# Kernel tuning notes

Hardware: AMD Instinct MI355X
Metric: run time of the kernel (lower is better)

Reference implementation:

```python
import jax, jax.numpy as jnp
import numpy as np

B, T, C, H = 8, 2048, 1024, 128  # batch, seq (== block_size), n_embd, head_size


def setup_inputs() -> dict:
    key = jax.random.key(0)
    ks = jax.random.split(key, 4)
    s = 1.0 / np.sqrt(C)  # keep logits sane for softmax
    return {
        "embedded_data": jax.random.normal(ks[0], (B, T, C), dtype=jnp.float32),
        "Wq": jax.random.normal(ks[1], (C, H), dtype=jnp.float32) * s,
        "bq": jnp.zeros((H,), dtype=jnp.float32),
        "Wk": jax.random.normal(ks[2], (C, H), dtype=jnp.float32) * s,
        "bk": jnp.zeros((H,), dtype=jnp.float32),
        "Wv": jax.random.normal(ks[3], (C, H), dtype=jnp.float32) * s,
        "bv": jnp.zeros((H,), dtype=jnp.float32),
    }


def reference(embedded_data, Wq, bq, Wk, bk, Wv, bv):
    Bc, Tc, Cc = embedded_data.shape
    q = embedded_data @ Wq + bq                      # [B,T,H]
    k = embedded_data @ Wk + bk                      # [B,T,H]
    v = embedded_data @ Wv + bv                      # [B,T,H]
    # NOTE: source scales by C**-0.5 (input embed dim), not head_size**-0.5
    wei = jnp.einsum("bqh,bkh->bqk", q, k) * (Cc ** -0.5)  # [B,T,T]
    causal = jnp.tril(jnp.ones((Tc, Tc), dtype=bool))
    wei = jnp.where(causal, wei, -jnp.inf)
    wei = jax.nn.softmax(wei, axis=-1)
    # dropout(p=0.2) is identity in eval mode
    out = jnp.einsum("bqk,bkh->bqh", wei, v)         # [B,T,H]
    return out
```

## Files before the change

### kernel.cpp

```cpp
#include <hip/hip_runtime.h>
#include <cstdint>
#include <cstddef>

typedef __bf16 bf16x8 __attribute__((ext_vector_type(8)));
typedef float f32x4 __attribute__((ext_vector_type(4)));

#define B_ 8
#define T_ 2048
#define C_ 1024
#define H_ 128

#define QSC 0.045084220027780106f

__device__ __forceinline__ unsigned short f2bf(float f) {
    __bf16 h = (__bf16)f;
    return *(unsigned short*)&h;
}
__device__ __forceinline__ float bf2f(unsigned short u) {
    union { unsigned int i; float f; } x; x.i = ((unsigned int)u) << 16;
    return x.f;
}

__device__ __forceinline__ void gload16(void* lds, const void* g) {
    __builtin_amdgcn_global_load_lds(
        (const __attribute__((address_space(1))) unsigned int*)g,
        (__attribute__((address_space(3))) unsigned int*)lds, 16, 0, 0);
}

__global__ __launch_bounds__(256) void prep_w(
    const float* __restrict__ Wq, const float* __restrict__ Wk,
    const float* __restrict__ Wv, unsigned short* __restrict__ wt)
{
    int gid = blockIdx.x * 256 + threadIdx.x;
    int which = gid >> 14;
    int rem = gid & 16383;
    int n = rem >> 7;
    int kc = rem & 127;
    const float* W = which == 0 ? Wq : (which == 1 ? Wk : Wv);
    unsigned short tmp[8];
    #pragma unroll
    for (int i = 0; i < 8; ++i) tmp[i] = f2bf(W[(size_t)(kc * 8 + i) * H_ + n]);
    *(uint4*)&wt[((size_t)which * H_ + n) * C_ + kc * 8] = *(uint4*)tmp;
}

__global__ __launch_bounds__(512, 2) void proj_fused(
    const float* __restrict__ x, const unsigned short* __restrict__ wt,
    const float* __restrict__ bq, const float* __restrict__ bk,
    const float* __restrict__ bv,
    unsigned short* __restrict__ qo, unsigned short* __restrict__ ko,
    unsigned short* __restrict__ vo)
{
    __shared__ float xs[2][64 * 64];
    __shared__ unsigned short ws2[2][384 * 64];

    const int tid = threadIdx.x;
    const int w = tid >> 6, l = tid & 63, gl = l >> 4, lc = l & 15;
    const int rb = (w >> 1) * 16;
    const int cb = (w & 1) * 192;
    const int m0 = blockIdx.x * 64;

    f32x4 acc[12];
    #pragma unroll
    for (int jn = 0; jn < 12; ++jn) acc[jn] = f32x4{0.f, 0.f, 0.f, 0.f};

    auto stage = [&](int buf, int kc2) {
        const int kb = kc2 * 64;
        #pragma unroll
        for (int ji = 0; ji < 6; ++ji) {
            int slot = ji * 512 + tid;
            int R = slot >> 3, cs = slot & 7;
            gload16(&ws2[buf][(ji * 512 + w * 64) * 8],
                    &wt[(size_t)R * C_ + kb + ((cs ^ (R & 7)) * 8)]);
        }
        #pragma unroll
        for (int ji = 0; ji < 2; ++ji) {
            int slot = ji * 512 + tid;
            int r = slot >> 4, cs = slot & 15;
            gload16(&xs[buf][(ji * 512 + w * 64) * 4],
                    &x[(size_t)(m0 + r) * C_ + kb + ((cs ^ (r & 15)) * 4)]);
        }
    };

    stage(0, 0);
    __syncthreads();

    int cur = 0;
    for (int kc = 0; kc < 16; ++kc) {
        if (kc < 15) stage(cur ^ 1, kc + 1);
        #pragma unroll
        for (int ks = 0; ks < 2; ++ks) {
            const int row = rb + lc;
            const int u0 = ks * 8 + gl * 2;
            f32x4 lo = *(const f32x4*)&xs[cur][(row * 16 + (u0 ^ (row & 15))) * 4];
            f32x4 hi = *(const f32x4*)&xs[cur][(row * 16 + ((u0 + 1) ^ (row & 15))) * 4];
            bf16x8 af;
            af[0] = (__bf16)lo[0]; af[1] = (__bf16)lo[1];
            af[2] = (__bf16)lo[2]; af[3] = (__bf16)lo[3];
            af[4] = (__bf16)hi[0]; af[5] = (__bf16)hi[1];
            af[6] = (__bf16)hi[2]; af[7] = (__bf16)hi[3];
            #pragma unroll
            for (int jn = 0; jn < 12; ++jn) {
                int R = cb + jn * 16 + lc;
                bf16x8 bfr = *(const bf16x8*)&ws2[cur][(R * 8 + ((ks * 4 + gl) ^ (R & 7))) * 8];
                acc[jn] = __builtin_amdgcn_mfma_f32_16x16x32_bf16(af, bfr, acc[jn], 0, 0, 0);
            }
        }
        __syncthreads();
        cur ^= 1;
    }

    unsigned short* eb = (unsigned short*)&ws2[0][0];
    #pragma unroll
    for (int jn = 0; jn < 12; ++jn) {
        int n = cb + jn * 16 + lc;
        int wh = n >> 7, nl = n & 127;
        float bb = (wh == 0) ? bq[nl] : (wh == 1 ? bk[nl] : bv[nl]);
        float sc = (wh == 0) ? QSC : 1.0f;
        #pragma unroll
        for (int r = 0; r < 4; ++r) {
            int row = rb + gl * 4 + r;
            eb[row * 392 + n] = f2bf((acc[jn][r] + bb) * sc);
        }
    }
    __syncthreads();

    const int bi = m0 >> 11, t0 = m0 & (T_ - 1);
    #pragma unroll
    for (int i = 0; i < 2; ++i) {
        int c = i * 512 + tid;
        {
            int row = c >> 4, c16 = c & 15;
            *(uint4*)&qo[(size_t)(m0 + row) * H_ + c16 * 8] =
                *(const uint4*)&eb[row * 392 + c16 * 8];
            *(uint4*)&ko[(size_t)(m0 + row) * H_ + c16 * 8] =
                *(const uint4*)&eb[row * 392 + 128 + c16 * 8];
        }
        {
            int n = c >> 3, cc = c & 7;
            unsigned short tmp[8];
            #pragma unroll
            for (int ii = 0; ii < 8; ++ii)
                tmp[ii] = eb[(cc * 8 + ii) * 392 + 256 + n];
            *(uint4*)&vo[((size_t)(bi * H_ + n)) * T_ + t0 + cc * 8] = *(uint4*)tmp;
        }
    }
}

__device__ __forceinline__ int pasc(int qt) {
    int m = qt >> 2, j = qt & 3;
    return 2 * m * (m + 1) + j * (m + 1);
}

__global__ __launch_bounds__(256, 2) void attn_split7(
    const unsigned short* __restrict__ q,
    const unsigned short* __restrict__ k,
    const unsigned short* __restrict__ vT,
    float* __restrict__ out,
    unsigned short* __restrict__ Opart, float* __restrict__ lws)
{
    const int bb = blockIdx.x;
    const int jj = 143 - (int)blockIdx.y;
    int qt = 31;
    while (pasc(qt) > jj) --qt;
    const int c = jj - pasc(qt);
    const int nch = (qt >> 2) + 1;
    const int q0 = qt * 64;
    const int kstart = c * 256;
    const int kend = min(kstart + 256, q0 + 64);
    const int ntiles = (kend - kstart) >> 5;

    const unsigned short* qb = q  + (size_t)bb * T_ * H_;
    const unsigned short* kb = k  + (size_t)bb * T_ * H_;
    const unsigned short* vb = vT + (size_t)bb * H_ * T_;

    __shared__ unsigned short Ks[2][32 * 128];
    __shared__ unsigned short Vs[2][128 * 32];
    __shared__ unsigned short Ps[4][16 * 64];

    const int tid = threadIdx.x;
    const int w = tid >> 6, l = tid & 63, gl = l >> 4, lc = l & 15;
    const int rowbase = q0 + w * 16;

    bf16x8 aq[4];
    #pragma unroll
    for (int ds = 0; ds < 4; ++ds)
        aq[ds] = *(const bf16x8*)&qb[(size_t)(rowbase + lc) * H_ + ds * 32 + gl * 8];

    f32x4 o[8];
    #pragma unroll
    for (int jo = 0; jo < 8; ++jo) o[jo] = f32x4{0.f, 0.f, 0.f, 0.f};
    float l_acc[4];
    #pragma unroll
    for (int r = 0; r < 4; ++r) l_acc[r] = 0.f;

    auto stageK = [&](int buf, int t) {
        const int kv0 = kstart + t * 32;
        #pragma unroll
        for (int ji = 0; ji < 2; ++ji) {
            int slot = (w * 2 + ji) * 64 + l;
            int r = slot >> 4, cs = slot & 15;
            gload16(&Ks[buf][((w * 2 + ji) * 64) * 8],
                    &kb[(size_t)(kv0 + r) * H_ + ((cs ^ (r & 7)) * 8)]);
        }
    };
    auto stageV = [&](int buf, int t) {
        const int kv0 = kstart + t * 32;
        #pragma unroll
        for (int ji = 0; ji < 2; ++ji) {
            int slot = (w * 2 + ji) * 64 + l;
            int r = slot >> 2, cs = slot & 3;
            gload16(&Vs[buf][((w * 2 + ji) * 64) * 8],
                    &vb[(size_t)r * T_ + kv0 + ((cs ^ (r & 3)) * 8)]);
        }
    };

    stageK(0, 0);
    stageV(0, 0);
    __syncthreads();

    int cur = 0;
    for (int t = 0; t < ntiles; ++t) {
        if (t + 1 < ntiles) { stageK(cur ^ 1, t + 1); stageV(cur ^ 1, t + 1); }
        const int kv0 = kstart + t * 32;
        const bool active = kv0 < rowbase + 16;
        if (active) {
            f32x4 s[2];
            #pragma unroll
            for (int jk = 0; jk < 2; ++jk) s[jk] = f32x4{0.f, 0.f, 0.f, 0.f};
            #pragma unroll
            for (int ds = 0; ds < 4; ++ds) {
                #pragma unroll
                for (int jk = 0; jk < 2; ++jk) {
                    int row = jk * 16 + lc;
                    bf16x8 kf = *(const bf16x8*)&Ks[cur][(row * 16 + ((ds * 4 + gl) ^ (row & 7))) * 8];
                    s[jk] = __builtin_amdgcn_mfma_f32_16x16x32_bf16(aq[ds], kf, s[jk], 0, 0, 0);
                }
            }
            if (kv0 + 31 > rowbase) {
                #pragma unroll
                for (int jk = 0; jk < 2; ++jk)
                    #pragma unroll
                    for (int r = 0; r < 4; ++r)
                        if (kv0 + jk * 16 + lc > rowbase + gl * 4 + r) s[jk][r] = -1e30f;
            }
            #pragma unroll
            for (int jk = 0; jk < 2; ++jk)
                #pragma unroll
                for (int r = 0; r < 4; ++r) {
                    float p = exp2f(fminf(s[jk][r], 80.f));
                    s[jk][r] = p;
                    l_acc[r] += p;
                }
            #pragma unroll
            for (int jk = 0; jk < 2; ++jk)
                #pragma unroll
                for (int r = 0; r < 4; ++r) {
                    int row = gl * 4 + r;
                    Ps[w][(row * 64 + jk * 16 + lc) ^ ((row & 7) << 3)] = f2bf(s[jk][r]);
                }
            {
                bf16x8 pa = *(const bf16x8*)&Ps[w][(lc * 64 + gl * 8) ^ ((lc & 7) << 3)];
                #pragma unroll
                for (int jo = 0; jo < 8; ++jo) {
                    int d = jo * 16 + lc;
                    bf16x8 vf = *(const bf16x8*)&Vs[cur][(d * 4 + (gl ^ (d & 3))) * 8];
                    o[jo] = __builtin_amdgcn_mfma_f32_16x16x32_bf16(pa, vf, o[jo], 0, 0, 0);
                }
            }
        }
        __syncthreads();
        cur ^= 1;
    }

    #pragma unroll
    for (int off = 1; off < 16; off <<= 1)
        #pragma unroll
        for (int r = 0; r < 4; ++r)
            l_acc[r] += __shfl_xor(l_acc[r], off, 64);

    if (nch == 1) {
        float* ob = out + (size_t)bb * T_ * H_;
        float inv[4];
        #pragma unroll
        for (int r = 0; r < 4; ++r) inv[r] = 1.0f / l_acc[r];
        #pragma unroll
        for (int jo = 0; jo < 8; ++jo)
            #pragma unroll
            for (int r = 0; r < 4; ++r)
                ob[(size_t)(rowbase + gl * 4 + r) * H_ + jo * 16 + lc] = o[jo][r] * inv[r];
    } else {
        const int slot = bb * 140 + (pasc(qt) - 4 + c);
        unsigned short* op = Opart + (size_t)slot * 8192;
        #pragma unroll
        for (int jo = 0; jo < 8; ++jo)
            #pragma unroll
            for (int r = 0; r < 4; ++r)
                op[(w * 16 + gl * 4 + r) * 128 + jo * 16 + lc] = f2bf(o[jo][r]);
        if (lc == 0) {
            #pragma unroll
            for (int r = 0; r < 4; ++r)
                lws[slot * 64 + w * 16 + gl * 4 + r] = l_acc[r];
        }
    }
}

__global__ __launch_bounds__(256) void combine_kernel(
    const unsigned short* __restrict__ Opart, const float* __restrict__ lws,
    float* __restrict__ out)
{
    const int rowid = blockIdx.x * 4 + (threadIdx.x >> 6);
    const int lane = threadIdx.x & 63;
    const int bb = rowid / 1792;
    const int t = 256 + (rowid - bb * 1792);
    const int qt = t >> 6;
    const int m = qt >> 2;
    const int nch = m + 1;
    const int p0 = 2 * m * (m + 1) + (qt & 3) * (m + 1);
    const int base = bb * 140 + (p0 - 4);
    const int r64 = t & 63;

    float L = 0.f, a0 = 0.f, a1 = 0.f;
    #pragma unroll
    for (int c2 = 0; c2 < 8; ++c2)
        if (c2 < nch) {
            L += lws[(base + c2) * 64 + r64];
            ushort2 uv = *(const ushort2*)&Opart[(size_t)(base + c2) * 8192 + r64 * 128 + lane * 2];
            a0 += bf2f(uv.x); a1 += bf2f(uv.y);
        }
    const float invL = 1.0f / L;
    *(float2*)&out[((size_t)bb * T_ + t) * H_ + lane * 2] = make_float2(a0 * invL, a1 * invL);
}

__global__ __launch_bounds__(128) void attn_mono(
    const unsigned short* __restrict__ q,
    const unsigned short* __restrict__ k,
    const unsigned short* __restrict__ vT,
    float* __restrict__ out)
{
    const int qt = (gridDim.x - 1) - blockIdx.x;
    const int bb = blockIdx.y;
    const int q0 = qt * 32;
    const unsigned short* qb = q  + (size_t)bb * T_ * H_;
    const unsigned short* kb = k  + (size_t)bb * T_ * H_;
    const unsigned short* vb = vT + (size_t)bb * H_ * T_;

    __shared__ unsigned short Ps[2][16 * 64];

    const int tid = threadIdx.x;
    const int w = tid >> 6, l = tid & 63, gl = l >> 4, lc = l & 15;

    bf16x8 aq[4];
    #pragma unroll
    for (int ds = 0; ds < 4; ++ds)
        aq[ds] = *(const bf16x8*)&qb[(size_t)(q0 + w * 16 + lc) * H_ + ds * 32 + gl * 8];

    f32x4 o[8];
    #pragma unroll
    for (int jo = 0; jo < 8; ++jo) o[jo] = f32x4{0.f, 0.f, 0.f, 0.f};
    float m_run[4], l_run[4];
    #pragma unroll
    for (int r = 0; r < 4; ++r) { m_run[r] = -INFINITY; l_run[r] = 0.f; }

    const int nt = (q0 >> 6) + 1;
    for (int t = 0; t < nt; ++t) {
        const int kv0 = t * 64;
        f32x4 s[4];
        #pragma unroll
        for (int jk = 0; jk < 4; ++jk) s[jk] = f32x4{0.f, 0.f, 0.f, 0.f};
        #pragma unroll
        for (int ds = 0; ds < 4; ++ds)
            #pragma unroll
            for (int jk = 0; jk < 4; ++jk) {
                bf16x8 bf = *(const bf16x8*)&kb[(size_t)(kv0 + jk * 16 + lc) * H_ + ds * 32 + gl * 8];
                s[jk] = __builtin_amdgcn_mfma_f32_16x16x32_bf16(aq[ds], bf, s[jk], 0, 0, 0);
            }
        if (kv0 + 63 > q0) {
            const int rowg = q0 + w * 16 + gl * 4;
            #pragma unroll
            for (int jk = 0; jk < 4; ++jk)
                #pragma unroll
                for (int r = 0; r < 4; ++r)
                    if (kv0 + jk * 16 + lc > rowg + r) s[jk][r] = -1e30f;
        }
        float pm[4];
        #pragma unroll
        for (int r = 0; r < 4; ++r)
            pm[r] = fmaxf(fmaxf(s[0][r], s[1][r]), fmaxf(s[2][r], s[3][r]));
        #pragma unroll
        for (int off = 1; off < 16; off <<= 1)
            #pragma unroll
            for (int r = 0; r < 4; ++r)
                pm[r] = fmaxf(pm[r], __shfl_xor(pm[r], off, 64));
        float scl[4], rs[4];
        #pragma unroll
        for (int r = 0; r < 4; ++r) {
            float mn = fmaxf(m_run[r], pm[r]);
            scl[r] = exp2f(m_run[r] - mn);
            m_run[r] = mn;
            rs[r] = 0.f;
        }
        #pragma unroll
        for (int jk = 0; jk < 4; ++jk)
            #pragma unroll
            for (int r = 0; r < 4; ++r) {
                float p = exp2f(s[jk][r] - m_run[r]);
                s[jk][r] = p;
                rs[r] += p;
            }
        #pragma unroll
        for (int off = 1; off < 16; off <<= 1)
            #pragma unroll
            for (int r = 0; r < 4; ++r)
                rs[r] += __shfl_xor(rs[r], off, 64);
        #pragma unroll
        for (int r = 0; r < 4; ++r)
            l_run[r] = l_run[r] * scl[r] + rs[r];
        #pragma unroll
        for (int jo = 0; jo < 8; ++jo)
            #pragma unroll
            for (int r = 0; r < 4; ++r)
                o[jo][r] *= scl[r];
        #pragma unroll
        for (int jk = 0; jk < 4; ++jk)
            #pragma unroll
            for (int r = 0; r < 4; ++r) {
                int row = gl * 4 + r;
                Ps[w][(row * 64 + jk * 16 + lc) ^ ((row & 7) << 3)] = f2bf(s[jk][r]);
            }
        #pragma unroll
        for (int ks = 0; ks < 2; ++ks) {
            bf16x8 pa = *(const bf16x8*)&Ps[w][(lc * 64 + ks * 32 + gl * 8) ^ ((lc & 7) << 3)];
            #pragma unroll
            for (int jo = 0; jo < 8; ++jo) {
                bf16x8 bv_ = *(const bf16x8*)&vb[(size_t)(jo * 16 + lc) * T_ + kv0 + ks * 32 + gl * 8];
                o[jo] = __builtin_amdgcn_mfma_f32_16x16x32_bf16(pa, bv_, o[jo], 0, 0, 0);
            }
        }
    }
    float* ob = out + (size_t)bb * T_ * H_;
    #pragma unroll
    for (int jo = 0; jo < 8; ++jo)
        #pragma unroll
        for (int r = 0; r < 4; ++r)
            ob[(size_t)(q0 + w * 16 + gl * 4 + r) * H_ + jo * 16 + lc] = o[jo][r] / l_run[r];
}

extern "C" void kernel_launch(void* const* d_in, const int* in_sizes, int n_in,
                              void* d_out, int out_size, void* d_ws, size_t ws_size,
                              hipStream_t stream) {
    const float* x  = (const float*)d_in[0];
    const float* Wq = (const float*)d_in[1];
    const float* bq = (const float*)d_in[2];
    const float* Wk = (const float*)d_in[3];
    const float* bk = (const float*)d_in[4];
    const float* Wv = (const float*)d_in[5];
    const float* bv = (const float*)d_in[6];
    float* out = (float*)d_out;

    const size_t qkv = (size_t)B_ * T_ * H_;
    unsigned short* qws = (unsigned short*)d_ws;
    unsigned short* kws = qws + qkv;
    unsigned short* vws = kws + qkv;
    unsigned short* wtw = vws + qkv;
    const size_t base_bytes = (3 * qkv + (size_t)3 * H_ * C_) * 2;
    unsigned short* Opart = (unsigned short*)((char*)d_ws + base_bytes);
    float* lws = (float*)((char*)d_ws + base_bytes + (size_t)1120 * 8192 * 2);
    const size_t need = base_bytes + (size_t)1120 * 8192 * 2 + (size_t)1120 * 64 * 4;

    prep_w<<<dim3(192), 256, 0, stream>>>(Wq, Wk, Wv, wtw);
    proj_fused<<<dim3(256), 512, 0, stream>>>(x, wtw, bq, bk, bv, qws, kws, vws);
    if (ws_size >= need) {
        attn_split7<<<dim3(8, 144), 256, 0, stream>>>(qws, kws, vws, out, Opart, lws);
        combine_kernel<<<dim3(3584), 256, 0, stream>>>(Opart, lws, out);
    } else {
        attn_mono<<<dim3(64, 8), 128, 0, stream>>>(qws, kws, vws, out);
    }
}
```

Baseline: 74.24 us.

## Retile projection GEMM to 6 waves each computing 64x64 output blocks

The QKV projection kernel moves from 8 waves, each owning a 16x192 strip, to 6 waves, each owning a full 64-row by 64-column tile with a 4x4 MFMA accumulator grid. Each wave now loads 4 A fragments and 4 B fragments per k-step for 16 MFMAs, instead of 1 A and 12 B for 12 MFMAs. The aim is to cut LDS reads per MFMA. The cost is redundant fp32-to-bf16 conversion of x in every wave, more accumulator registers, and fewer waves to hide latency. Staging and epilogue loops are rebalanced for 384 threads.

```diff
diff --git a/kernel.cpp b/kernel.cpp
--- a/kernel.cpp
+++ b/kernel.cpp
@@ -43,7 +43,7 @@
     *(uint4*)&wt[((size_t)which * H_ + n) * C_ + kc * 8] = *(uint4*)tmp;
 }
 
-__global__ __launch_bounds__(512, 2) void proj_fused(
+__global__ __launch_bounds__(384, 2) void proj_fused2(
     const float* __restrict__ x, const unsigned short* __restrict__ wt,
     const float* __restrict__ bq, const float* __restrict__ bk,
     const float* __restrict__ bv,
@@ -55,29 +55,32 @@
 
     const int tid = threadIdx.x;
     const int w = tid >> 6, l = tid & 63, gl = l >> 4, lc = l & 15;
-    const int rb = (w >> 1) * 16;
-    const int cb = (w & 1) * 192;
+    const int cb = w * 64;
     const int m0 = blockIdx.x * 64;
 
-    f32x4 acc[12];
-    #pragma unroll
-    for (int jn = 0; jn < 12; ++jn) acc[jn] = f32x4{0.f, 0.f, 0.f, 0.f};
+    f32x4 acc[4][4];
+    #pragma unroll
+    for (int im = 0; im < 4; ++im)
+        #pragma unroll
+        for (int jn = 0; jn < 4; ++jn) acc[im][jn] = f32x4{0.f, 0.f, 0.f, 0.f};
 
     auto stage = [&](int buf, int kc2) {
         const int kb = kc2 * 64;
-        #pragma unroll
-        for (int ji = 0; ji < 6; ++ji) {
-            int slot = ji * 512 + tid;
+        if (w < 4) {
+            #pragma unroll
+            for (int ji = 0; ji < 4; ++ji) {
+                int slot = ji * 256 + tid;
+                int r = slot >> 4, cs = slot & 15;
+                gload16(&xs[buf][(ji * 256 + w * 64) * 4],
+                        &x[(size_t)(m0 + r) * C_ + kb + ((cs ^ (r & 15)) * 4)]);
+            }
+        }
+        #pragma unroll
+        for (int ji = 0; ji < 8; ++ji) {
+            int slot = ji * 384 + tid;
             int R = slot >> 3, cs = slot & 7;
-            gload16(&ws2[buf][(ji * 512 + w * 64) * 8],
+            gload16(&ws2[buf][(ji * 384 + w * 64) * 8],
                     &wt[(size_t)R * C_ + kb + ((cs ^ (R & 7)) * 8)]);
-        }
-        #pragma unroll
-        for (int ji = 0; ji < 2; ++ji) {
-            int slot = ji * 512 + tid;
-            int r = slot >> 4, cs = slot & 15;
-            gload16(&xs[buf][(ji * 512 + w * 64) * 4],
-                    &x[(size_t)(m0 + r) * C_ + kb + ((cs ^ (r & 15)) * 4)]);
         }
     };
 
@@ -89,21 +92,31 @@
         if (kc < 15) stage(cur ^ 1, kc + 1);
         #pragma unroll
         for (int ks = 0; ks < 2; ++ks) {
-            const int row = rb + lc;
+            bf16x8 a[4], b[4];
             const int u0 = ks * 8 + gl * 2;
-            f32x4 lo = *(const f32x4*)&xs[cur][(row * 16 + (u0 ^ (row & 15))) * 4];
-            f32x4 hi = *(const f32x4*)&xs[cur][(row * 16 + ((u0 + 1) ^ (row & 15))) * 4];
-            bf16x8 af;
-            af[0] = (__bf16)lo[0]; af[1] = (__bf16)lo[1];
-            af[2] = (__bf16)lo[2]; af[3] = (__bf16)lo[3];
-            af[4] = (__bf16)hi[0]; af[5] = (__bf16)hi[1];
-            af[6] = (__bf16)hi[2]; af[7] = (__bf16)hi[3];
-            #pragma unroll
-            for (int jn = 0; jn < 12; ++jn) {
+            #pragma unroll
+            for (int im = 0; im < 4; ++im) {
+                int row = im * 16 + lc;
+                f32x4 lo = *(const f32x4*)&xs[cur][(row * 16 + (u0 ^ (row & 15))) * 4];
+                f32x4 hi = *(const f32x4*)&xs[cur][(row * 16 + ((u0 + 1) ^ (row & 15))) * 4];
+                bf16x8 af;
+                af[0] = (__bf16)lo[0]; af[1] = (__bf16)lo[1];
+                af[2] = (__bf16)lo[2]; af[3] = (__bf16)lo[3];
+                af[4] = (__bf16)hi[0]; af[5] = (__bf16)hi[1];
+                af[6] = (__bf16)hi[2]; af[7] = (__bf16)hi[3];
+                a[im] = af;
+            }
+            #pragma unroll
+            for (int jn = 0; jn < 4; ++jn) {
                 int R = cb + jn * 16 + lc;
-                bf16x8 bfr = *(const bf16x8*)&ws2[cur][(R * 8 + ((ks * 4 + gl) ^ (R & 7))) * 8];
-                acc[jn] = __builtin_amdgcn_mfma_f32_16x16x32_bf16(af, bfr, acc[jn], 0, 0, 0);
-            }
+                b[jn] = *(const bf16x8*)&ws2[cur][(R * 8 + ((ks * 4 + gl) ^ (R & 7))) * 8];
+            }
+            #pragma unroll
+            for (int im = 0; im < 4; ++im)
+                #pragma unroll
+                for (int jn = 0; jn < 4; ++jn)
+                    acc[im][jn] = __builtin_amdgcn_mfma_f32_16x16x32_bf16(
+                        a[im], b[jn], acc[im][jn], 0, 0, 0);
         }
         __syncthreads();
         cur ^= 1;
@@ -111,37 +124,41 @@
 
     unsigned short* eb = (unsigned short*)&ws2[0][0];
     #pragma unroll
-    for (int jn = 0; jn < 12; ++jn) {
+    for (int jn = 0; jn < 4; ++jn) {
         int n = cb + jn * 16 + lc;
         int wh = n >> 7, nl = n & 127;
         float bb = (wh == 0) ? bq[nl] : (wh == 1 ? bk[nl] : bv[nl]);
         float sc = (wh == 0) ? QSC : 1.0f;
         #pragma unroll
-        for (int r = 0; r < 4; ++r) {
-            int row = rb + gl * 4 + r;
-            eb[row * 392 + n] = f2bf((acc[jn][r] + bb) * sc);
-        }
+        for (int im = 0; im < 4; ++im)
+            #pragma unroll
+            for (int r = 0; r < 4; ++r) {
+                int row = im * 16 + gl * 4 + r;
+                eb[row * 392 + n] = f2bf((acc[im][jn][r] + bb) * sc);
+            }
     }
     __syncthreads();
 
     const int bi = m0 >> 11, t0 = m0 & (T_ - 1);
     #pragma unroll
-    for (int i = 0; i < 2; ++i) {
-        int c = i * 512 + tid;
-        {
-            int row = c >> 4, c16 = c & 15;
-            *(uint4*)&qo[(size_t)(m0 + row) * H_ + c16 * 8] =
-                *(const uint4*)&eb[row * 392 + c16 * 8];
-            *(uint4*)&ko[(size_t)(m0 + row) * H_ + c16 * 8] =
-                *(const uint4*)&eb[row * 392 + 128 + c16 * 8];
-        }
-        {
-            int n = c >> 3, cc = c & 7;
-            unsigned short tmp[8];
-            #pragma unroll
-            for (int ii = 0; ii < 8; ++ii)
-                tmp[ii] = eb[(cc * 8 + ii) * 392 + 256 + n];
-            *(uint4*)&vo[((size_t)(bi * H_ + n)) * T_ + t0 + cc * 8] = *(uint4*)tmp;
+    for (int i = 0; i < 3; ++i) {
+        int c = i * 384 + tid;
+        if (c < 1024) {
+            {
+                int row = c >> 4, c16 = c & 15;
+                *(uint4*)&qo[(size_t)(m0 + row) * H_ + c16 * 8] =
+                    *(const uint4*)&eb[row * 392 + c16 * 8];
+                *(uint4*)&ko[(size_t)(m0 + row) * H_ + c16 * 8] =
+                    *(const uint4*)&eb[row * 392 + 128 + c16 * 8];
+            }
+            {
+                int n = c >> 3, cc = c & 7;
+                unsigned short tmp[8];
+                #pragma unroll
+                for (int ii = 0; ii < 8; ++ii)
+                    tmp[ii] = eb[(cc * 8 + ii) * 392 + 256 + n];
+                *(uint4*)&vo[((size_t)(bi * H_ + n)) * T_ + t0 + cc * 8] = *(uint4*)tmp;
+            }
         }
     }
 }
@@ -468,7 +485,7 @@
     const size_t need = base_bytes + (size_t)1120 * 8192 * 2 + (size_t)1120 * 64 * 4;
 
     prep_w<<<dim3(192), 256, 0, stream>>>(Wq, Wk, Wv, wtw);
-    proj_fused<<<dim3(256), 512, 0, stream>>>(x, wtw, bq, bk, bv, qws, kws, vws);
+    proj_fused2<<<dim3(256), 384, 0, stream>>>(x, wtw, bq, bk, bv, qws, kws, vws);
     if (ws_size >= need) {
         attn_split7<<<dim3(8, 144), 256, 0, stream>>>(qws, kws, vws, out, Opart, lws);
         combine_kernel<<<dim3(3584), 256, 0, stream>>>(Opart, lws, out);
```

Result: slower. 78.30 us (+5.5%).
